# Performance work log

Hardware: AMD Instinct MI355X
Metric: run time of the kernel (lower is better)

Reference implementation:

```python
import jax, jax.numpy as jnp
import numpy as np

B, S, D, H = 2, 2048, 1024, 16


def setup_inputs() -> dict:
    key = jax.random.key(0)
    kq, kk, kv, kw = jax.random.split(key, 4)
    Q = jax.random.normal(kq, (B, S, D), dtype=jnp.float32)
    K = jax.random.normal(kk, (B, S, D), dtype=jnp.float32)
    V = jax.random.normal(kv, (B, S, D), dtype=jnp.float32)
    Wo = jax.random.normal(kw, (D, D), dtype=jnp.float32) * (1.0 / np.sqrt(D))
    return {"Q": Q, "K": K, "V": V, "Wo": Wo, "num_heads": H}


def reference(Q, K, V, Wo, num_heads):
    b, s, d = Q.shape
    dk = d // num_heads
    # split heads: [B,S,D] -> [B,H,S,dk]
    q = Q.reshape(b, s, num_heads, dk).transpose(0, 2, 1, 3)
    k = K.reshape(b, s, num_heads, dk).transpose(0, 2, 1, 3)
    v = V.reshape(b, s, num_heads, dk).transpose(0, 2, 1, 3)
    scale = 1.0 / jnp.sqrt(jnp.asarray(dk, dtype=q.dtype))
    logits = jnp.einsum('bhqd,bhkd->bhqk', q, k) * scale  # [B,H,S,S]
    probs = jax.nn.softmax(logits, axis=-1).astype(q.dtype)
    o = jnp.einsum('bhqk,bhkd->bhqd', probs, v)  # [B,H,S,dk]
    o = o.transpose(0, 2, 1, 3).reshape(b, s, d)  # concat heads
    # O = einsum('d dkh, ... dkh -> ... d', Wo, scores) == scores @ Wo^T
    return jnp.einsum('dk,bsk->bsd', Wo, o)
```

## Files before the change

kernel.cpp:

```cpp
#include <hip/hip_runtime.h>
#include <hip/hip_bf16.h>

#define B_ 2
#define S_ 2048
#define D_ 1024
#define H_ 16
#define DK_ 64

typedef __hip_bfloat16 bf16;
typedef short v8s __attribute__((ext_vector_type(8)));
typedef short v4s __attribute__((ext_vector_type(4)));
typedef float v4f __attribute__((ext_vector_type(4)));
typedef float v16f __attribute__((ext_vector_type(16)));
typedef int   v4i __attribute__((ext_vector_type(4)));
typedef int   v2i __attribute__((ext_vector_type(2)));

static __device__ __forceinline__ v16f mfma32(v8s a, v8s b, v16f c) {
  return __builtin_amdgcn_mfma_f32_32x32x16_bf16(a, b, c, 0, 0, 0);
}
static __device__ __forceinline__ void gl2lds16(const void* g, void* l) {
  __builtin_amdgcn_global_load_lds((const __attribute__((address_space(1))) void*)g,
                                   (__attribute__((address_space(3))) void*)l,
                                   16, 0, 0);
}
static __device__ __forceinline__ short f2bf(float x) {
  return (short)__builtin_bit_cast(unsigned short, __float2bfloat16(x));
}
static __device__ __forceinline__ int pk2f(float lo, float hi) {
  unsigned a = __builtin_bit_cast(unsigned, lo) + 0x8000u;
  unsigned b = __builtin_bit_cast(unsigned, hi) + 0x8000u;
  return (int)__builtin_amdgcn_perm(b, a, 0x07060302u);
}
static __device__ __forceinline__ float bf2f(short s) {
  return __builtin_bit_cast(float, ((unsigned)(unsigned short)s) << 16);
}

__global__ __launch_bounds__(256) void pre_kernel(
    const float* __restrict__ K, const float* __restrict__ V,
    const float* __restrict__ Wo, bf16* __restrict__ Kb,
    bf16* __restrict__ Vt, bf16* __restrict__ Wb)
{
  __shared__ __align__(16) bf16 td[64 * 72];
  const int t = threadIdx.x;
  const int bx = blockIdx.x;

  if (bx < 2048) {
    const int idx = bx * 256 + t;
    const int seg = idx & 7;
    const int rest = idx >> 3;
    const int h = rest & 15;
    const int bs = rest >> 4;
    const float* src = K + (size_t)bs * D_ + h * 64 + seg * 8;
    v4f x = *(const v4f*)src, y = *(const v4f*)(src + 4);
    v8s r;
    r[0]=f2bf(x[0]); r[1]=f2bf(x[1]); r[2]=f2bf(x[2]); r[3]=f2bf(x[3]);
    r[4]=f2bf(y[0]); r[5]=f2bf(y[1]); r[6]=f2bf(y[2]); r[7]=f2bf(y[3]);
    const int b = bs >> 11, s = bs & 2047;
    *(v8s*)(Kb + ((size_t)(b * H_ + h) * S_ + s) * DK_ + seg * 8) = r;
  } else if (bx < 3072) {
    const int idx = bx - 2048;
    const int bh = idx >> 5, b = bh >> 4, h = bh & 15;
    const int s0 = (idx & 31) * 64;
    const int srow = t >> 2;
    const int cs = t & 3;
    const float* vp = V + (size_t)(b * S_ + s0 + srow) * D_ + h * 64 + cs * 16;
#pragma unroll
    for (int j = 0; j < 4; j++) {
      v4f x = *(const v4f*)(vp + j * 4);
#pragma unroll
      for (int jj = 0; jj < 4; jj++)
        td[(cs * 16 + j * 4 + jj) * 72 + srow] = __float2bfloat16(x[jj]);
    }
    __syncthreads();
    const int d = t >> 2;
#pragma unroll
    for (int a2 = 0; a2 < 4; a2++) {
      const int pos = cs * 16 + a2 * 4;
      const int g = pos >> 5;
      const int a = (pos >> 2) & 7;
      const int kbase = g * 32 + ((a >> 2) << 4) + ((a & 1) << 3) + (((a >> 1) & 1) << 2);
      v4s val = *(const v4s*)(td + d * 72 + kbase);
      *(v4s*)(Vt + ((size_t)bh * DK_ + d) * S_ + s0 + pos) = val;
    }
  } else {
    const int i = ((bx - 3072) * 256 + t) * 4;
    v4f a = *(const v4f*)(Wo + i);
    v4s r;
    r[0]=f2bf(a[0]); r[1]=f2bf(a[1]); r[2]=f2bf(a[2]); r[3]=f2bf(a[3]);
    *(v4s*)((short*)Wb + i) = r;
  }
}

__global__ __launch_bounds__(256, 4) void attn4_kernel(
    const float* __restrict__ Q, const bf16* __restrict__ Kb,
    const bf16* __restrict__ Vt, bf16* __restrict__ Op0,
    bf16* __restrict__ Op1, float* __restrict__ Lp)
{
  __shared__ __align__(16) bf16 kk[2][64 * 64];
  __shared__ __align__(16) bf16 vv[2][64 * 64];

  const int t = threadIdx.x;
  const int w = t >> 6, l = t & 63, h2 = l >> 5, ln = l & 31;
  const int bh = blockIdx.x, b = bh >> 4, h = bh & 15;
  const int qbase = blockIdx.y * 128 + w * 32;
  const int z = blockIdx.z;
  const int kb0 = z << 10;

  const bf16* Kbh = Kb + (size_t)bh * (S_ * DK_);
  const bf16* Vbh = Vt + (size_t)bh * (DK_ * S_);

  const float sc = 0.18033688011112042f;
  v8s bq[4];
  {
    const float* qp = Q + ((size_t)b * S_ + qbase + ln) * D_ + h * DK_ + h2 * 8;
#pragma unroll
    for (int c = 0; c < 4; c++) {
      v4f x = *(const v4f*)(qp + c * 16);
      v4f y = *(const v4f*)(qp + c * 16 + 4);
      v4i r = { pk2f(x[0]*sc, x[1]*sc), pk2f(x[2]*sc, x[3]*sc),
                pk2f(y[0]*sc, y[1]*sc), pk2f(y[2]*sc, y[3]*sc) };
      bq[c] = __builtin_bit_cast(v8s, r);
    }
  }

  v16f accA, accB;
#pragma unroll
  for (int r = 0; r < 16; r++) { accA[r] = 0.f; accB[r] = 0.f; }
  float lpart = 0.f;

#pragma unroll
  for (int j = 0; j < 2; j++) {
    const int flat = j * 256 + t, row = flat >> 3, sp = flat & 7;
    gl2lds16(Kbh + (size_t)(kb0 + row) * DK_ + ((sp ^ (row & 7)) * 8), &kk[0][flat * 8]);
    gl2lds16(Vbh + (size_t)row * S_ + kb0 + ((sp ^ (row & 7)) * 8), &vv[0][flat * 8]);
  }

  int it = 0;
  for (int kb = kb0; kb < kb0 + 1024; kb += 64, it ^= 1) {
    __syncthreads();
    if (kb + 64 < kb0 + 1024) {
#pragma unroll
      for (int j = 0; j < 2; j++) {
        const int flat = j * 256 + t, row = flat >> 3, sp = flat & 7;
        gl2lds16(Kbh + (size_t)(kb + 64 + row) * DK_ + ((sp ^ (row & 7)) * 8),
                 &kk[it ^ 1][flat * 8]);
        gl2lds16(Vbh + (size_t)row * S_ + (kb + 64) + ((sp ^ (row & 7)) * 8),
                 &vv[it ^ 1][flat * 8]);
      }
    }
    const bf16* kc_ = kk[it];
    const bf16* vc_ = vv[it];

    v16f s0, s1;
#pragma unroll
    for (int r = 0; r < 16; r++) { s0[r] = 0.f; s1[r] = 0.f; }
#pragma unroll
    for (int c = 0; c < 4; c++) {
      const int sd = 2 * c + h2;
      v8s a0 = *(const v8s*)(kc_ + ln * 64 + ((sd ^ (ln & 7)) * 8));
      v8s a1 = *(const v8s*)(kc_ + (32 + ln) * 64 + ((sd ^ (ln & 7)) * 8));
      s0 = mfma32(a0, bq[c], s0);
      s1 = mfma32(a1, bq[c], s1);
    }

    float p0[16], p1[16];
#pragma unroll
    for (int r = 0; r < 16; r++) { p0[r] = exp2f(s0[r]); p1[r] = exp2f(s1[r]); }
    float su = 0.f;
#pragma unroll
    for (int r = 0; r < 16; r++) su += p0[r] + p1[r];
    lpart += su;

    v4i i00 = { pk2f(p0[0],p0[1]),  pk2f(p0[2],p0[3]),  pk2f(p0[4],p0[5]),  pk2f(p0[6],p0[7]) };
    v4i i01 = { pk2f(p0[8],p0[9]),  pk2f(p0[10],p0[11]),pk2f(p0[12],p0[13]),pk2f(p0[14],p0[15]) };
    v4i i10 = { pk2f(p1[0],p1[1]),  pk2f(p1[2],p1[3]),  pk2f(p1[4],p1[5]),  pk2f(p1[6],p1[7]) };
    v4i i11 = { pk2f(p1[8],p1[9]),  pk2f(p1[10],p1[11]),pk2f(p1[12],p1[13]),pk2f(p1[14],p1[15]) };
    v8s pb00 = __builtin_bit_cast(v8s, i00);
    v8s pb01 = __builtin_bit_cast(v8s, i01);
    v8s pb10 = __builtin_bit_cast(v8s, i10);
    v8s pb11 = __builtin_bit_cast(v8s, i11);

#pragma unroll
    for (int st = 0; st < 2; st++) {
#pragma unroll
      for (int kc = 0; kc < 2; kc++) {
        const int q = st * 4 + kc * 2 + h2;
        v8s avA = *(const v8s*)(vc_ + ln * 64 + ((q ^ (ln & 7)) * 8));
        v8s avB = *(const v8s*)(vc_ + (32 + ln) * 64 + ((q ^ (ln & 7)) * 8));
        v8s pb = st ? (kc ? pb11 : pb10) : (kc ? pb01 : pb00);
        accA = mfma32(avA, pb, accA);
        accB = mfma32(avB, pb, accB);
      }
    }
  }

  __syncthreads();
  const float lfull = lpart + __shfl_xor(lpart, 32);
  const float linv = 1.0f / lfull;
  bf16* epw = &kk[0][0] + w * 2048;
#pragma unroll
  for (int r = 0; r < 16; r += 4) {
    const int off = 4 * h2;
    const int sgA = (r >> 2) ^ (ln & 3);
    const int sgB = 4 + sgA;
    v2i pa = { pk2f(accA[r]*linv,   accA[r+1]*linv),
               pk2f(accA[r+2]*linv, accA[r+3]*linv) };
    v2i pb = { pk2f(accB[r]*linv,   accB[r+1]*linv),
               pk2f(accB[r+2]*linv, accB[r+3]*linv) };
    *(v2i*)(epw + ln * 64 + sgA * 8 + off) = pa;
    *(v2i*)(epw + ln * 64 + sgB * 8 + off) = pb;
  }
  if (h2 == 0)
    Lp[((size_t)z * 32 + bh) * S_ + qbase + ln] = lfull;

  bf16* Op = z ? Op1 : Op0;
#pragma unroll
  for (int i = 0; i < 4; i++) {
    const int flat = i * 64 + l;
    const int qr = flat >> 3, sd = flat & 7;
    const int phys = ((sd & 3) ^ (qr & 3)) | (sd & 4);
    v8s val = *(const v8s*)(epw - w * 2048 + (w * 32 + qr) * 64 + phys * 8);
    *(v8s*)(Op + ((size_t)b * S_ + qbase - w * 32 + w * 32 + qr) * D_ + h * DK_ + sd * 8) = val;
  }
}

__global__ __launch_bounds__(256) void merge_kernel(
    const bf16* __restrict__ Op0, const bf16* __restrict__ Op1,
    const float* __restrict__ Lp, bf16* __restrict__ O)
{
  const int flat = blockIdx.x * 256 + threadIdx.x;
  const int qrow = flat >> 7;
  const int seg = flat & 127;
  const int b = qrow >> 11, s = qrow & 2047;
  const int h = seg >> 3;
  const int bh = b * H_ + h;
  const float l0 = Lp[(size_t)bh * S_ + s];
  const float l1 = Lp[(size_t)(32 + bh) * S_ + s];
  const float inv = 1.0f / (l0 + l1);
  const float w0 = l0 * inv, w1 = l1 * inv;
  const size_t off = (size_t)qrow * D_ + seg * 8;
  v8s a = *(const v8s*)(Op0 + off);
  v8s c = *(const v8s*)(Op1 + off);
  v4i r;
#pragma unroll
  for (int j = 0; j < 4; j++) {
    float lo = w0 * bf2f(a[2*j])   + w1 * bf2f(c[2*j]);
    float hi = w0 * bf2f(a[2*j+1]) + w1 * bf2f(c[2*j+1]);
    r[j] = pk2f(lo, hi);
  }
  *(v8s*)(O + off) = __builtin_bit_cast(v8s, r);
}

__global__ __launch_bounds__(256, 4) void proj3_kernel(
    const bf16* __restrict__ A, const bf16* __restrict__ Wo, float* __restrict__ Out)
{
  __shared__ __align__(16) bf16 aa[2][64 * 64];
  __shared__ __align__(16) bf16 bb[2][64 * 64];

  const int t = threadIdx.x;
  const int w = t >> 6, l = t & 63, h2 = l >> 5, ln = l & 31;
  const int m0 = blockIdx.x * 64, n0 = blockIdx.y * 64;
  const int wm = (w & 1) * 32, wn = (w >> 1) * 32;

  v16f acc;
#pragma unroll
  for (int r = 0; r < 16; r++) acc[r] = 0.f;

#pragma unroll
  for (int j = 0; j < 2; j++) {
    const int flat = j * 256 + t, row = flat >> 3, sp = flat & 7;
    gl2lds16(A  + (size_t)(m0 + row) * D_ + ((sp ^ (row & 7)) * 8), &aa[0][flat * 8]);
    gl2lds16(Wo + (size_t)(n0 + row) * D_ + ((sp ^ (row & 7)) * 8), &bb[0][flat * 8]);
  }

  int it = 0;
  for (int k0 = 0; k0 < D_; k0 += 64, it ^= 1) {
    __syncthreads();
    if (k0 + 64 < D_) {
#pragma unroll
      for (int j = 0; j < 2; j++) {
        const int flat = j * 256 + t, row = flat >> 3, sp = flat & 7;
        gl2lds16(A  + (size_t)(m0 + row) * D_ + (k0 + 64) + ((sp ^ (row & 7)) * 8),
                 &aa[it ^ 1][flat * 8]);
        gl2lds16(Wo + (size_t)(n0 + row) * D_ + (k0 + 64) + ((sp ^ (row & 7)) * 8),
                 &bb[it ^ 1][flat * 8]);
      }
    }
    const bf16* ac = aa[it];
    const bf16* bc = bb[it];
#pragma unroll
    for (int c = 0; c < 4; c++) {
      const int sd = 2 * c + h2;
      v8s av = *(const v8s*)(ac + (wm + ln) * 64 + ((sd ^ (ln & 7)) * 8));
      v8s bv = *(const v8s*)(bc + (wn + ln) * 64 + ((sd ^ (ln & 7)) * 8));
      acc = mfma32(av, bv, acc);
    }
  }

#pragma unroll
  for (int r = 0; r < 16; r++) {
    const int row = m0 + wm + (r & 3) + 4 * h2 + 8 * (r >> 2);
    Out[(size_t)row * D_ + n0 + wn + ln] = acc[r];
  }
}

extern "C" void kernel_launch(void* const* d_in, const int* in_sizes, int n_in,
                              void* d_out, int out_size, void* d_ws, size_t ws_size,
                              hipStream_t stream) {
  (void)in_sizes; (void)n_in; (void)out_size; (void)ws_size;
  const float* Q  = (const float*)d_in[0];
  const float* K  = (const float*)d_in[1];
  const float* V  = (const float*)d_in[2];
  const float* Wo = (const float*)d_in[3];
  float* out = (float*)d_out;

  bf16* base = (bf16*)d_ws;
  bf16* kb   = base;
  bf16* vt   = base + (size_t)4  * 1024 * 1024;
  bf16* wo_b = base + (size_t)8  * 1024 * 1024;
  bf16* op0  = base + (size_t)9  * 1024 * 1024;
  bf16* op1  = base + (size_t)13 * 1024 * 1024;
  float* lp  = (float*)(base + (size_t)17 * 1024 * 1024);
  bf16* ows  = kb;

  pre_kernel  <<<dim3(4096),       256, 0, stream>>>(K, V, Wo, kb, vt, wo_b);
  attn4_kernel<<<dim3(32, 16, 2),  256, 0, stream>>>(Q, kb, vt, op0, op1, lp);
  merge_kernel<<<dim3(2048),       256, 0, stream>>>(op0, op1, lp, ows);
  proj3_kernel<<<dim3(64, 16),     256, 0, stream>>>(ows, wo_b, out);
}
```

Before: 176.8 us.

## Fuse split-KV merge into output projection and drop per-split normalization

Removes the separate merge kernel. The projection kernel now loads both unnormalized split partial outputs plus the row sums, combines them as (a+c)/(l0+l1), and writes the bf16 result into LDS, software-pipelined with the Wo loads. The attention kernel no longer divides by its local sum, and its first QK MFMA takes a zero accumulator directly. This saves one launch and one full intermediate round trip through global memory. In exchange, each projection tile rereads Op0/Op1 once per N-block (16 times), and the register-staged loads replace the direct global-to-LDS path for A.

```diff
diff --git a/kernel.cpp b/kernel.cpp
--- a/kernel.cpp
+++ b/kernel.cpp
@@ -123,6 +123,10 @@
     }
   }
 
+  v16f Z;
+#pragma unroll
+  for (int r = 0; r < 16; r++) Z[r] = 0.f;
+
   v16f accA, accB;
 #pragma unroll
   for (int r = 0; r < 16; r++) { accA[r] = 0.f; accB[r] = 0.f; }
@@ -153,23 +157,26 @@
 
     v16f s0, s1;
 #pragma unroll
-    for (int r = 0; r < 16; r++) { s0[r] = 0.f; s1[r] = 0.f; }
-#pragma unroll
     for (int c = 0; c < 4; c++) {
       const int sd = 2 * c + h2;
       v8s a0 = *(const v8s*)(kc_ + ln * 64 + ((sd ^ (ln & 7)) * 8));
       v8s a1 = *(const v8s*)(kc_ + (32 + ln) * 64 + ((sd ^ (ln & 7)) * 8));
-      s0 = mfma32(a0, bq[c], s0);
-      s1 = mfma32(a1, bq[c], s1);
+      if (c == 0) {
+        s0 = mfma32(a0, bq[0], Z);
+        s1 = mfma32(a1, bq[0], Z);
+      } else {
+        s0 = mfma32(a0, bq[c], s0);
+        s1 = mfma32(a1, bq[c], s1);
+      }
     }
 
     float p0[16], p1[16];
 #pragma unroll
     for (int r = 0; r < 16; r++) { p0[r] = exp2f(s0[r]); p1[r] = exp2f(s1[r]); }
-    float su = 0.f;
-#pragma unroll
-    for (int r = 0; r < 16; r++) su += p0[r] + p1[r];
-    lpart += su;
+    float suA = 0.f, suB = 0.f;
+#pragma unroll
+    for (int r = 0; r < 16; r++) { suA += p0[r]; suB += p1[r]; }
+    lpart += suA + suB;
 
     v4i i00 = { pk2f(p0[0],p0[1]),  pk2f(p0[2],p0[3]),  pk2f(p0[4],p0[5]),  pk2f(p0[6],p0[7]) };
     v4i i01 = { pk2f(p0[8],p0[9]),  pk2f(p0[10],p0[11]),pk2f(p0[12],p0[13]),pk2f(p0[14],p0[15]) };
@@ -196,17 +203,16 @@
 
   __syncthreads();
   const float lfull = lpart + __shfl_xor(lpart, 32);
-  const float linv = 1.0f / lfull;
   bf16* epw = &kk[0][0] + w * 2048;
 #pragma unroll
   for (int r = 0; r < 16; r += 4) {
     const int off = 4 * h2;
     const int sgA = (r >> 2) ^ (ln & 3);
     const int sgB = 4 + sgA;
-    v2i pa = { pk2f(accA[r]*linv,   accA[r+1]*linv),
-               pk2f(accA[r+2]*linv, accA[r+3]*linv) };
-    v2i pb = { pk2f(accB[r]*linv,   accB[r+1]*linv),
-               pk2f(accB[r+2]*linv, accB[r+3]*linv) };
+    v2i pa = { pk2f(accA[r],   accA[r+1]),
+               pk2f(accA[r+2], accA[r+3]) };
+    v2i pb = { pk2f(accB[r],   accB[r+1]),
+               pk2f(accB[r+2], accB[r+3]) };
     *(v2i*)(epw + ln * 64 + sgA * 8 + off) = pa;
     *(v2i*)(epw + ln * 64 + sgB * 8 + off) = pb;
   }
@@ -224,35 +230,10 @@
   }
 }
 
-__global__ __launch_bounds__(256) void merge_kernel(
+__global__ __launch_bounds__(256, 4) void projm_kernel(
     const bf16* __restrict__ Op0, const bf16* __restrict__ Op1,
-    const float* __restrict__ Lp, bf16* __restrict__ O)
-{
-  const int flat = blockIdx.x * 256 + threadIdx.x;
-  const int qrow = flat >> 7;
-  const int seg = flat & 127;
-  const int b = qrow >> 11, s = qrow & 2047;
-  const int h = seg >> 3;
-  const int bh = b * H_ + h;
-  const float l0 = Lp[(size_t)bh * S_ + s];
-  const float l1 = Lp[(size_t)(32 + bh) * S_ + s];
-  const float inv = 1.0f / (l0 + l1);
-  const float w0 = l0 * inv, w1 = l1 * inv;
-  const size_t off = (size_t)qrow * D_ + seg * 8;
-  v8s a = *(const v8s*)(Op0 + off);
-  v8s c = *(const v8s*)(Op1 + off);
-  v4i r;
-#pragma unroll
-  for (int j = 0; j < 4; j++) {
-    float lo = w0 * bf2f(a[2*j])   + w1 * bf2f(c[2*j]);
-    float hi = w0 * bf2f(a[2*j+1]) + w1 * bf2f(c[2*j+1]);
-    r[j] = pk2f(lo, hi);
-  }
-  *(v8s*)(O + off) = __builtin_bit_cast(v8s, r);
-}
-
-__global__ __launch_bounds__(256, 4) void proj3_kernel(
-    const bf16* __restrict__ A, const bf16* __restrict__ Wo, float* __restrict__ Out)
+    const float* __restrict__ Lp, const bf16* __restrict__ Wo,
+    float* __restrict__ Out)
 {
   __shared__ __align__(16) bf16 aa[2][64 * 64];
   __shared__ __align__(16) bf16 bb[2][64 * 64];
@@ -261,27 +242,60 @@
   const int w = t >> 6, l = t & 63, h2 = l >> 5, ln = l & 31;
   const int m0 = blockIdx.x * 64, n0 = blockIdx.y * 64;
   const int wm = (w & 1) * 32, wn = (w >> 1) * 32;
+  const int b = m0 >> 11;
 
   v16f acc;
 #pragma unroll
   for (int r = 0; r < 16; r++) acc[r] = 0.f;
 
+  auto stage_load = [&](int k0, int j, v8s& a, v8s& c, float& inv) {
+    const int flat = j * 256 + t, row = flat >> 3, sp = flat & 7;
+    const int m = m0 + row, s = m & 2047;
+    const int h = k0 >> 6;
+    const size_t off = (size_t)m * D_ + k0 + ((sp ^ (row & 7)) * 8);
+    a = *(const v8s*)(Op0 + off);
+    c = *(const v8s*)(Op1 + off);
+    const float l0 = Lp[(size_t)(b * H_ + h) * S_ + s];
+    const float l1 = Lp[(size_t)(32 + b * H_ + h) * S_ + s];
+    inv = 1.0f / (l0 + l1);
+  };
+  auto stage_write = [&](int buf, int j, v8s a, v8s c, float inv) {
+    const int flat = j * 256 + t;
+    v4i A = __builtin_bit_cast(v4i, a), C = __builtin_bit_cast(v4i, c);
+    v4i r;
+#pragma unroll
+    for (int jj = 0; jj < 4; jj++) {
+      const unsigned aw = (unsigned)A[jj], cw = (unsigned)C[jj];
+      const float alo = __builtin_bit_cast(float, aw << 16);
+      const float ahi = __builtin_bit_cast(float, aw & 0xffff0000u);
+      const float clo = __builtin_bit_cast(float, cw << 16);
+      const float chi = __builtin_bit_cast(float, cw & 0xffff0000u);
+      r[jj] = pk2f((alo + clo) * inv, (ahi + chi) * inv);
+    }
+    *(v4i*)(&aa[buf][flat * 8]) = r;
+  };
+
+  v8s a0v, c0v, a1v, c1v; float i0v, i1v;
+  stage_load(0, 0, a0v, c0v, i0v);
+  stage_load(0, 1, a1v, c1v, i1v);
 #pragma unroll
   for (int j = 0; j < 2; j++) {
     const int flat = j * 256 + t, row = flat >> 3, sp = flat & 7;
-    gl2lds16(A  + (size_t)(m0 + row) * D_ + ((sp ^ (row & 7)) * 8), &aa[0][flat * 8]);
     gl2lds16(Wo + (size_t)(n0 + row) * D_ + ((sp ^ (row & 7)) * 8), &bb[0][flat * 8]);
   }
+  stage_write(0, 0, a0v, c0v, i0v);
+  stage_write(0, 1, a1v, c1v, i1v);
 
   int it = 0;
   for (int k0 = 0; k0 < D_; k0 += 64, it ^= 1) {
     __syncthreads();
-    if (k0 + 64 < D_) {
+    const bool nxt = (k0 + 64 < D_);
+    if (nxt) {
+      stage_load(k0 + 64, 0, a0v, c0v, i0v);
+      stage_load(k0 + 64, 1, a1v, c1v, i1v);
 #pragma unroll
       for (int j = 0; j < 2; j++) {
         const int flat = j * 256 + t, row = flat >> 3, sp = flat & 7;
-        gl2lds16(A  + (size_t)(m0 + row) * D_ + (k0 + 64) + ((sp ^ (row & 7)) * 8),
-                 &aa[it ^ 1][flat * 8]);
         gl2lds16(Wo + (size_t)(n0 + row) * D_ + (k0 + 64) + ((sp ^ (row & 7)) * 8),
                  &bb[it ^ 1][flat * 8]);
       }
@@ -294,6 +308,10 @@
       v8s av = *(const v8s*)(ac + (wm + ln) * 64 + ((sd ^ (ln & 7)) * 8));
       v8s bv = *(const v8s*)(bc + (wn + ln) * 64 + ((sd ^ (ln & 7)) * 8));
       acc = mfma32(av, bv, acc);
+    }
+    if (nxt) {
+      stage_write(it ^ 1, 0, a0v, c0v, i0v);
+      stage_write(it ^ 1, 1, a1v, c1v, i1v);
     }
   }
 
@@ -321,10 +339,8 @@
   bf16* op0  = base + (size_t)9  * 1024 * 1024;
   bf16* op1  = base + (size_t)13 * 1024 * 1024;
   float* lp  = (float*)(base + (size_t)17 * 1024 * 1024);
-  bf16* ows  = kb;
 
   pre_kernel  <<<dim3(4096),       256, 0, stream>>>(K, V, Wo, kb, vt, wo_b);
   attn4_kernel<<<dim3(32, 16, 2),  256, 0, stream>>>(Q, kb, vt, op0, op1, lp);
-  merge_kernel<<<dim3(2048),       256, 0, stream>>>(op0, op1, lp, ows);
-  proj3_kernel<<<dim3(64, 16),     256, 0, stream>>>(ows, wo_b, out);
-}
+  projm_kernel<<<dim3(64, 16),     256, 0, stream>>>(op0, op1, lp, wo_b, out);
+}
```

Measured after the change: 178.8 us. About the same (+1.1%).
